# Optimization experiments

Measured on AMD Instinct MI355X. Metric: run time of the kernel, lower is better.

Reference implementation:

```python
import jax, jax.numpy as jnp
import numpy as np

N = 50000
E = 800000
IN_FEAT = 128
HEADS = 2
HEAD_DIM = 64  # hidden_feat // num_heads for 'concat'
HIDDEN = HEADS * HEAD_DIM
N_CLASSES = 16
NEG_SLOPE = 0.2
BN_EPS = 1e-5


def setup_inputs() -> dict:
    key = jax.random.key(0)
    ks = jax.random.split(key, 20)
    s = 0.1  # weight scale for numerical sanity
    return {
        "x": jax.random.normal(ks[0], (N, IN_FEAT), jnp.float32),
        "src0": jax.random.randint(ks[1], (E,), 0, N, jnp.int32),
        "dst0": jax.random.randint(ks[2], (E,), 0, N, jnp.int32),
        "ew0": jax.random.uniform(ks[3], (E,), jnp.float32),
        "src1": jax.random.randint(ks[4], (E,), 0, N, jnp.int32),
        "dst1": jax.random.randint(ks[5], (E,), 0, N, jnp.int32),
        "ew1": jax.random.uniform(ks[6], (E,), jnp.float32),
        "fc_w0": jax.random.normal(ks[7], (HIDDEN, IN_FEAT), jnp.float32) * s,
        "bias0": jnp.zeros((HIDDEN,), jnp.float32),
        "attn_l0": jax.random.normal(ks[8], (HEADS, HEAD_DIM), jnp.float32) * s,
        "attn_r0": jax.random.normal(ks[9], (HEADS, HEAD_DIM), jnp.float32) * s,
        "fc_w1": jax.random.normal(ks[10], (HIDDEN, IN_FEAT), jnp.float32) * s,
        "bias1": jnp.zeros((HIDDEN,), jnp.float32),
        "attn_l1": jax.random.normal(ks[11], (HEADS, HEAD_DIM), jnp.float32) * s,
        "attn_r1": jax.random.normal(ks[12], (HEADS, HEAD_DIM), jnp.float32) * s,
        "skip_w": jax.random.normal(ks[13], (HIDDEN, IN_FEAT), jnp.float32) * s,
        "skip_b": jnp.zeros((HIDDEN,), jnp.float32),
        "bn_gamma": jnp.ones((HIDDEN,), jnp.float32),
        "bn_beta": jnp.zeros((HIDDEN,), jnp.float32),
        "clf_w": jax.random.normal(ks[14], (N_CLASSES, HIDDEN), jnp.float32) * s,
        "clf_b": jnp.zeros((N_CLASSES,), jnp.float32),
    }


def _weighted_gat(x, src, dst, ew, fc_w, bias, attn_l, attn_r):
    # DGL GATConv with per-edge weight scaling of attention.
    f = (x @ fc_w.T).reshape(N, HEADS, HEAD_DIM)          # [N,H,D]
    el = jnp.sum(f * attn_l, axis=-1)                      # [N,H]
    er = jnp.sum(f * attn_r, axis=-1)                      # [N,H]
    e = jax.nn.leaky_relu(el[src] + er[dst], NEG_SLOPE)    # [E,H]
    # edge softmax over incoming edges of each dst, numerically stable
    m = jax.ops.segment_max(e, dst, num_segments=N)        # [N,H]
    ex = jnp.exp(e - m[dst])
    den = jax.ops.segment_sum(ex, dst, num_segments=N)     # [N,H]
    alpha = ex / den[dst]                                  # [E,H]
    alpha = alpha * ew[:, None]                            # edge-weight scaling
    msg = alpha[..., None] * f[src]                        # [E,H,D]
    out = jax.ops.segment_sum(msg, dst, num_segments=N)    # [N,H,D]
    return out + bias.reshape(1, HEADS, HEAD_DIM)


def reference(x, src0, dst0, ew0, src1, dst1, ew1,
              fc_w0, bias0, attn_l0, attn_r0,
              fc_w1, bias1, attn_l1, attn_r1,
              skip_w, skip_b, bn_gamma, bn_beta, clf_w, clf_b):
    # HeteroGraphConv with aggregate='sum': sum per-relation GAT outputs
    h2 = _weighted_gat(x, src0, dst0, ew0, fc_w0, bias0, attn_l0, attn_r0) \
       + _weighted_gat(x, src1, dst1, ew1, fc_w1, bias1, attn_l1, attn_r1)
    # multihead 'concat' aggregate with relu: flatten heads
    h2 = jax.nn.relu(h2).reshape(N, HIDDEN)
    # linear skip + residual add (dropout is identity at eval)
    h = (x @ skip_w.T + skip_b) + h2
    # classifier: BatchNorm1d (batch stats) -> ReLU -> Linear
    mu = jnp.mean(h, axis=0)
    var = jnp.mean((h - mu) ** 2, axis=0)
    hn = (h - mu) * jax.lax.rsqrt(var + BN_EPS) * bn_gamma + bn_beta
    logits = jax.nn.relu(hn) @ clf_w.T + clf_b
    return logits
```

## Files before the change

### kernel.cpp

```cpp
#include <hip/hip_runtime.h>
#include <hip/hip_bf16.h>

#define N_NODES 50000
#define N_EDGES 800000
#define HID 128
#define NEG_SLOPE 0.2f
#define BN_EPS 1e-5f

#define NBLK 256
#define BINSZ 512
#define BINSH 9
#define NBINS 98

typedef __bf16 v8bf __attribute__((ext_vector_type(8)));
typedef float v4f __attribute__((ext_vector_type(4)));

__device__ __forceinline__ float leaky(float v) {
    return (v > 0.f) ? v : v * NEG_SLOPE;
}
__device__ __forceinline__ unsigned int f2bu(float f) {
    __hip_bfloat16 b = __float2bfloat16(f);
    return (unsigned int)*reinterpret_cast<unsigned short*>(&b);
}
__device__ __forceinline__ unsigned int pack2bf(float lo, float hi) {
    return f2bu(lo) | (f2bu(hi) << 16);
}

__global__ __launch_bounds__(256) void k_prepw(const float* __restrict__ w0,
                                               const float* __restrict__ w1,
                                               const float* __restrict__ wsk,
                                               unsigned short* __restrict__ wb) {
    const int WQ = 128 * 128 / 4;
    int q = blockIdx.x * 256 + threadIdx.x;
    if (q >= 3 * WQ) return;
    int mat = q >> 12;
    int rem = q & 4095;
    const float* W = (mat == 0) ? w0 : (mat == 1) ? w1 : wsk;
    float4 v = ((const float4*)W)[rem];
    ushort4 o;
    o.x = (unsigned short)f2bu(v.x);
    o.y = (unsigned short)f2bu(v.y);
    o.z = (unsigned short)f2bu(v.z);
    o.w = (unsigned short)f2bu(v.w);
    *(ushort4*)(wb + (size_t)mat * 16384 + rem * 4) = o;
}

__global__ __launch_bounds__(256) void k_bincount(const int* __restrict__ dst0,
                                                  const int* __restrict__ dst1,
                                                  int* __restrict__ bincnt) {
    int rel = blockIdx.y;
    const int* dst = rel ? dst1 : dst0;
    __shared__ int cnt[NBINS];
    for (int i = threadIdx.x; i < NBINS; i += 256) cnt[i] = 0;
    __syncthreads();
    const int CH = (N_EDGES + NBLK - 1) / NBLK;
    int b0 = blockIdx.x * CH;
    int b1 = min(N_EDGES, b0 + CH);
    for (int e = b0 + threadIdx.x; e < b1; e += 256)
        atomicAdd(&cnt[dst[e] >> BINSH], 1);
    __syncthreads();
    for (int i = threadIdx.x; i < NBINS; i += 256)
        bincnt[rel * NBINS * NBLK + i * NBLK + blockIdx.x] = cnt[i];
}

__global__ __launch_bounds__(1024) void k_binscan(int* __restrict__ bincnt) {
    int* a = bincnt + blockIdx.x * NBINS * NBLK;
    const int TOT = NBINS * NBLK;
    const int CH = (TOT + 1023) / 1024;
    int tid = threadIdx.x;
    int base = tid * CH;
    int lv[CH];
    int sum = 0;
    for (int i = 0; i < CH; i++) {
        int idx = base + i;
        int v = (idx < TOT) ? a[idx] : 0;
        lv[i] = sum;
        sum += v;
    }
    __shared__ int ls[1024];
    ls[tid] = sum;
    __syncthreads();
    for (int ofs = 1; ofs < 1024; ofs <<= 1) {
        int v = (tid >= ofs) ? ls[tid - ofs] : 0;
        __syncthreads();
        ls[tid] += v;
        __syncthreads();
    }
    int pre = tid ? ls[tid - 1] : 0;
    for (int i = 0; i < CH; i++) {
        int idx = base + i;
        if (idx < TOT) a[idx] = pre + lv[i];
    }
}

__global__ __launch_bounds__(256) void k_binscatter(const int* __restrict__ dst0,
                                                    const int* __restrict__ dst1,
                                                    const int* __restrict__ src0,
                                                    const int* __restrict__ src1,
                                                    const float* __restrict__ ew0,
                                                    const float* __restrict__ ew1,
                                                    const int* __restrict__ bincnt,
                                                    int2* __restrict__ pairs0,
                                                    int2* __restrict__ pairs1) {
    int rel = blockIdx.y;
    const int* dst = rel ? dst1 : dst0;
    const int* src = rel ? src1 : src0;
    const float* ew = rel ? ew1 : ew0;
    int2* pairs = rel ? pairs1 : pairs0;
    __shared__ int cur[NBINS];
    for (int i = threadIdx.x; i < NBINS; i += 256)
        cur[i] = bincnt[rel * NBINS * NBLK + i * NBLK + blockIdx.x];
    __syncthreads();
    const int CH = (N_EDGES + NBLK - 1) / NBLK;
    int b0 = blockIdx.x * CH;
    int b1 = min(N_EDGES, b0 + CH);
    for (int e = b0 + threadIdx.x; e < b1; e += 256) {
        int d = dst[e];
        int pos = atomicAdd(&cur[d >> BINSH], 1);
        unsigned int packed = (unsigned int)(d & (BINSZ - 1)) |
                              ((unsigned int)src[e] << BINSH);
        pairs[pos] = make_int2((int)packed, __float_as_int(ew[e]));
    }
}

__global__ __launch_bounds__(256) void k_csr(const int* __restrict__ bincnt,
                                             const int2* __restrict__ pairs0,
                                             const int2* __restrict__ pairs1,
                                             const float* __restrict__ el0,
                                             const float* __restrict__ el1,
                                             int* __restrict__ offs0,
                                             int* __restrict__ offs1,
                                             int4* __restrict__ rec0,
                                             int4* __restrict__ rec1) {
    int rel = blockIdx.y;
    const int2* pairs = rel ? pairs1 : pairs0;
    const float* el = rel ? el1 : el0;
    int* offs = rel ? offs1 : offs0;
    int4* rec = rel ? rec1 : rec0;
    int bin = blockIdx.x;
    int tid = threadIdx.x;
    const int* bc = bincnt + rel * NBINS * NBLK;
    int pbase = bc[bin * NBLK];
    int pend = (bin < NBINS - 1) ? bc[(bin + 1) * NBLK] : N_EDGES;
    int n0 = bin << BINSH;
    int nn = min(N_NODES - n0, BINSZ);

    __shared__ int s_deg[BINSZ];
    __shared__ int s_ts[256];
    for (int i = tid; i < BINSZ; i += 256) s_deg[i] = 0;
    __syncthreads();
    for (int p = pbase + tid; p < pend; p += 256)
        atomicAdd(&s_deg[((unsigned int)pairs[p].x) & (BINSZ - 1)], 1);
    __syncthreads();

    int d0 = s_deg[tid * 2], d1 = s_deg[tid * 2 + 1];
    s_ts[tid] = d0 + d1;
    __syncthreads();
    for (int ofs = 1; ofs < 256; ofs <<= 1) {
        int v = (tid >= ofs) ? s_ts[tid - ofs] : 0;
        __syncthreads();
        s_ts[tid] += v;
        __syncthreads();
    }
    int pre = tid ? s_ts[tid - 1] : 0;
    s_deg[tid * 2] = pbase + pre;
    s_deg[tid * 2 + 1] = pbase + pre + d0;
    __syncthreads();

    for (int l = tid; l < nn; l += 256) offs[n0 + l] = s_deg[l];
    if (bin == NBINS - 1 && tid == 0) offs[N_NODES] = N_EDGES;
    __syncthreads();

    for (int p = pbase + tid; p < pend; p += 256) {
        int2 pr = pairs[p];
        unsigned int u = (unsigned int)pr.x;
        int dl = (int)(u & (BINSZ - 1));
        int s = (int)(u >> BINSH);
        int pos = atomicAdd(&s_deg[dl], 1);
        float2 ev = *(const float2*)(el + 2 * s);
        rec[pos] = make_int4(s << 8, pr.y,
                             __float_as_int(ev.x), __float_as_int(ev.y));
    }
}

__global__ __launch_bounds__(256) void k_gemm_mfma(
    const float* __restrict__ x, const unsigned short* __restrict__ wb,
    const float* __restrict__ skip_b,
    const float* __restrict__ al0, const float* __restrict__ ar0,
    const float* __restrict__ al1, const float* __restrict__ ar1,
    unsigned short* __restrict__ fb0, unsigned short* __restrict__ fb1,
    float* __restrict__ el0, float* __restrict__ er0,
    float* __restrict__ el1, float* __restrict__ er1,
    float* __restrict__ hs) {
    __shared__ unsigned short As[64][128];
    __shared__ unsigned short Bs[64][128];
    int tid = threadIdx.x;
    int m0 = blockIdx.x * 64;

#pragma unroll
    for (int i = 0; i < 4; i++) {
        int idx = tid * 4 + i;
        int row = idx >> 4, seg = idx & 15;
        int gr = m0 + row;
        uint4 o = make_uint4(0, 0, 0, 0);
        if (gr < N_NODES) {
            const float* p = x + (size_t)gr * HID + seg * 8;
            float4 p0 = *(const float4*)p;
            float4 p1 = *(const float4*)(p + 4);
            o.x = pack2bf(p0.x, p0.y);
            o.y = pack2bf(p0.z, p0.w);
            o.z = pack2bf(p1.x, p1.y);
            o.w = pack2bf(p1.z, p1.w);
        }
        *(uint4*)(&As[row][(seg ^ (row & 7)) * 8]) = o;
    }
    __syncthreads();

    int w = tid >> 6, l = tid & 63;
    int lr = l & 15, lg = l >> 4;
    int arow = w * 16 + lr;
    v8bf afrag[4];
#pragma unroll
    for (int kb = 0; kb < 4; kb++)
        afrag[kb] = *(v8bf*)(&As[arow][((kb * 4 + lg) ^ (arow & 7)) * 8]);

    for (int s = 0; s < 6; s++) {
        int mat = s >> 1;
        int j0 = (s & 1) * 64;
        const unsigned short* wmat = wb + (size_t)mat * 16384 + j0 * HID;
        __syncthreads();
#pragma unroll
        for (int i = 0; i < 4; i++) {
            int idx = tid * 4 + i;
            int row = idx >> 4, seg = idx & 15;
            uint4 wv = *(const uint4*)(wmat + row * HID + seg * 8);
            *(uint4*)(&Bs[row][(seg ^ (row & 7)) * 8]) = wv;
        }
        __syncthreads();

        v4f acc[4] = {};
#pragma unroll
        for (int nt = 0; nt < 4; nt++) {
            int brow = nt * 16 + lr;
#pragma unroll
            for (int kb = 0; kb < 4; kb++) {
                v8bf bfrag =
                    *(v8bf*)(&Bs[brow][((kb * 4 + lg) ^ (brow & 7)) * 8]);
                acc[nt] = __builtin_amdgcn_mfma_f32_16x16x32_bf16(
                    afrag[kb], bfrag, acc[nt], 0, 0, 0);
            }
        }

        if (mat < 2) {
            int h = s & 1;
            const float* al = mat ? al1 : al0;
            const float* ar = mat ? ar1 : ar0;
            float* elp = mat ? el1 : el0;
            float* erp = mat ? er1 : er0;
            unsigned short* fbp = mat ? fb1 : fb0;
            float elv[4] = {0.f, 0.f, 0.f, 0.f};
            float erv[4] = {0.f, 0.f, 0.f, 0.f};
#pragma unroll
            for (int nt = 0; nt < 4; nt++) {
                int colg = j0 + nt * 16 + lr;
                float av = al[colg], rv = ar[colg];
#pragma unroll
                for (int r = 0; r < 4; r++) {
                    elv[r] += acc[nt][r] * av;
                    erv[r] += acc[nt][r] * rv;
                }
            }
#pragma unroll
            for (int m = 1; m < 16; m <<= 1)
#pragma unroll
                for (int r = 0; r < 4; r++) {
                    elv[r] += __shfl_xor(elv[r], m);
                    erv[r] += __shfl_xor(erv[r], m);
                }
#pragma unroll
            for (int r = 0; r < 4; r++) {
                int grow = m0 + w * 16 + lg * 4 + r;
                if (grow >= N_NODES) continue;
#pragma unroll
                for (int nt = 0; nt < 4; nt++) {
                    int colg = j0 + nt * 16 + lr;
                    fbp[(size_t)grow * HID + colg] =
                        (unsigned short)f2bu(acc[nt][r]);
                }
                if (lr == 0) {
                    elp[grow * 2 + h] = elv[r];
                    erp[grow * 2 + h] = erv[r];
                }
            }
        } else {
#pragma unroll
            for (int r = 0; r < 4; r++) {
                int grow = m0 + w * 16 + lg * 4 + r;
                if (grow >= N_NODES) continue;
#pragma unroll
                for (int nt = 0; nt < 4; nt++) {
                    int colg = j0 + nt * 16 + lr;
                    hs[(size_t)grow * HID + colg] = acc[nt][r] + skip_b[colg];
                }
            }
        }
    }
}

__device__ __forceinline__ void agg_rel2(const int* __restrict__ offs,
                                         const int4* __restrict__ rec,
                                         const float* __restrict__ er,
                                         const unsigned char* __restrict__ fbb,
                                         int n, int lane, int sub,
                                         int hh, float* a) {
    int b = offs[n];
    int e_end = offs[n + 1];
    int deg = e_end - b;
    if (deg <= 0) return;
    float ern0 = er[2 * n], ern1 = er[2 * n + 1];

    const int NC = 4;
    int cs[NC];
    float cw0[NC], cw1[NC];
    unsigned int cpk[NC];
    float d0 = 0.f, d1 = 0.f;
    int nchunk = (deg + 63) >> 6;
    for (int ch = 0; ch < nchunk; ch++) {
        int p = b + (ch << 6) + lane;
        int s = 0;
        float w0 = 0.f, w1 = 0.f;
        if (p < e_end) {
            int4 r = rec[p];
            s = r.x;
            float wgt = __int_as_float(r.y);
            float x0 = expf(leaky(__int_as_float(r.z) + ern0));
            float x1 = expf(leaky(__int_as_float(r.w) + ern1));
            d0 += x0;
            d1 += x1;
            w0 = x0 * wgt;
            w1 = x1 * wgt;
        }
        if (ch < NC) {
            cs[ch] = s;
            cw0[ch] = w0;
            cw1[ch] = w1;
        }
    }
#pragma unroll
    for (int m = 32; m; m >>= 1) {
        d0 += __shfl_xor(d0, m);
        d1 += __shfl_xor(d1, m);
    }
    float inv0 = 1.f / d0, inv1 = 1.f / d1;
#pragma unroll
    for (int ch = 0; ch < NC; ch++)
        cpk[ch] = pack2bf(cw0[ch] * inv0, cw1[ch] * inv1);

    for (int ch = 0; ch < nchunk; ch++) {
        int s;
        unsigned int pk;
        if (ch < NC) {
            s = cs[ch];
            pk = cpk[ch];
        } else {
            int p = b + (ch << 6) + lane;
            s = 0;
            pk = 0;
            if (p < e_end) {
                int4 r = rec[p];
                s = r.x;
                float wgt = __int_as_float(r.y);
                float w0 = expf(leaky(__int_as_float(r.z) + ern0)) * wgt;
                float w1 = expf(leaky(__int_as_float(r.w) + ern1)) * wgt;
                pk = pack2bf(w0 * inv0, w1 * inv1);
            }
        }
        int cnt = deg - (ch << 6);
        if (cnt > 64) cnt = 64;
        int ng = (cnt + 3) >> 2;
#pragma unroll 2
        for (int g = 0; g < ng; g++) {
            int sl = (g << 2) + sub;
            int sj = __shfl(s, sl);
            unsigned int pkj = (unsigned int)__shfl((int)pk, sl);
            float aj = __uint_as_float(hh ? (pkj & 0xffff0000u) : (pkj << 16));
            uint4 fv = *(const uint4*)(fbb + sj);
            a[0] += aj * __uint_as_float(fv.x << 16);
            a[1] += aj * __uint_as_float(fv.x & 0xffff0000u);
            a[2] += aj * __uint_as_float(fv.y << 16);
            a[3] += aj * __uint_as_float(fv.y & 0xffff0000u);
            a[4] += aj * __uint_as_float(fv.z << 16);
            a[5] += aj * __uint_as_float(fv.z & 0xffff0000u);
            a[6] += aj * __uint_as_float(fv.w << 16);
            a[7] += aj * __uint_as_float(fv.w & 0xffff0000u);
        }
    }
}

__global__ __launch_bounds__(256) void k_aggregate(
    const int* __restrict__ offs0, const int4* __restrict__ rec0,
    const float* __restrict__ er0, const unsigned short* __restrict__ fb0,
    const int* __restrict__ offs1, const int4* __restrict__ rec1,
    const float* __restrict__ er1, const unsigned short* __restrict__ fb1,
    const float* __restrict__ bias0, const float* __restrict__ bias1,
    float* __restrict__ h) {
    int wave = threadIdx.x >> 6, lane = threadIdx.x & 63;
    int n = blockIdx.x * 4 + wave;
    if (n >= N_NODES) return;
    int cb = lane & 15;
    int sub = lane >> 4;
    int hh = cb >> 3;
    float a[8] = {0.f, 0.f, 0.f, 0.f, 0.f, 0.f, 0.f, 0.f};
    const unsigned char* fbb0 = (const unsigned char*)fb0 + cb * 16;
    const unsigned char* fbb1 = (const unsigned char*)fb1 + cb * 16;
    agg_rel2(offs0, rec0, er0, fbb0, n, lane, sub, hh, a);
    agg_rel2(offs1, rec1, er1, fbb1, n, lane, sub, hh, a);
#pragma unroll
    for (int j = 0; j < 8; j++) {
        a[j] += __shfl_xor(a[j], 16);
        a[j] += __shfl_xor(a[j], 32);
    }
    if (sub == 0) {
        size_t base = (size_t)n * HID + cb * 8;
        float4 v0 = *(const float4*)(h + base);
        float4 v1 = *(const float4*)(h + base + 4);
        int c0 = cb * 8;
        float4 o0, o1;
        o0.x = v0.x + fmaxf(a[0] + bias0[c0 + 0] + bias1[c0 + 0], 0.f);
        o0.y = v0.y + fmaxf(a[1] + bias0[c0 + 1] + bias1[c0 + 1], 0.f);
        o0.z = v0.z + fmaxf(a[2] + bias0[c0 + 2] + bias1[c0 + 2], 0.f);
        o0.w = v0.w + fmaxf(a[3] + bias0[c0 + 3] + bias1[c0 + 3], 0.f);
        o1.x = v1.x + fmaxf(a[4] + bias0[c0 + 4] + bias1[c0 + 4], 0.f);
        o1.y = v1.y + fmaxf(a[5] + bias0[c0 + 5] + bias1[c0 + 5], 0.f);
        o1.z = v1.z + fmaxf(a[6] + bias0[c0 + 6] + bias1[c0 + 6], 0.f);
        o1.w = v1.w + fmaxf(a[7] + bias0[c0 + 7] + bias1[c0 + 7], 0.f);
        *(float4*)(h + base) = o0;
        *(float4*)(h + base + 4) = o1;
    }
}

__global__ __launch_bounds__(256) void k_bnstats(const float* __restrict__ h,
                                                 double* __restrict__ psum,
                                                 double* __restrict__ psumsq) {
    int tid = threadIdx.x;
    const float4* h4 = (const float4*)h;
    double s[4] = {0.0, 0.0, 0.0, 0.0};
    double q[4] = {0.0, 0.0, 0.0, 0.0};
    const int totalv = N_NODES * HID / 4;
    const int stride = 512 * 256;
    for (int i = blockIdx.x * 256 + tid; i < totalv; i += stride) {
        float4 v = h4[i];
        s[0] += v.x; q[0] += (double)v.x * v.x;
        s[1] += v.y; q[1] += (double)v.y * v.y;
        s[2] += v.z; q[2] += (double)v.z * v.z;
        s[3] += v.w; q[3] += (double)v.w * v.w;
    }
    __shared__ double ls[256][4], lq[256][4];
#pragma unroll
    for (int j = 0; j < 4; j++) {
        ls[tid][j] = s[j];
        lq[tid][j] = q[j];
    }
    __syncthreads();
    if (tid < 32) {
#pragma unroll
        for (int j = 0; j < 4; j++) {
            double ss = 0.0, qq = 0.0;
            for (int t = tid; t < 256; t += 32) {
                ss += ls[t][j];
                qq += lq[t][j];
            }
            psum[blockIdx.x * 128 + tid * 4 + j] = ss;
            psumsq[blockIdx.x * 128 + tid * 4 + j] = qq;
        }
    }
}

__global__ void k_bn_finalize(const double* __restrict__ psum,
                              const double* __restrict__ psumsq,
                              const float* __restrict__ gamma,
                              const float* __restrict__ beta,
                              float* __restrict__ ss) {
    int c = threadIdx.x;
    double s = 0.0, q = 0.0;
    for (int b = 0; b < 512; b++) {
        s += psum[b * 128 + c];
        q += psumsq[b * 128 + c];
    }
    double mu = s / N_NODES;
    double var = q / N_NODES - mu * mu;
    float sc = gamma[c] * (float)(1.0 / sqrt(var + (double)BN_EPS));
    ss[c] = sc;
    ss[128 + c] = beta[c] - (float)mu * sc;
}

__global__ __launch_bounds__(256) void k_classify(const float* __restrict__ h,
                                                  const float* __restrict__ ss,
                                                  const float* __restrict__ clf_w,
                                                  const float* __restrict__ clf_b,
                                                  float* __restrict__ out) {
    int w = threadIdx.x >> 6, l = threadIdx.x & 63;
    int lr = l & 15, lg = l >> 4;
    int n0 = (blockIdx.x * 4 + w) * 16;
    if (n0 >= N_NODES) return;

    v8bf afrag[4], bfrag[4];
#pragma unroll
    for (int kb = 0; kb < 4; kb++) {
        int k0 = kb * 32 + lg * 8;
        const float* bp = clf_w + lr * HID + k0;
        float4 b0 = *(const float4*)bp;
        float4 b1 = *(const float4*)(bp + 4);
        bfrag[kb][0] = (__bf16)b0.x; bfrag[kb][1] = (__bf16)b0.y;
        bfrag[kb][2] = (__bf16)b0.z; bfrag[kb][3] = (__bf16)b0.w;
        bfrag[kb][4] = (__bf16)b1.x; bfrag[kb][5] = (__bf16)b1.y;
        bfrag[kb][6] = (__bf16)b1.z; bfrag[kb][7] = (__bf16)b1.w;
        const float* ap = h + (size_t)(n0 + lr) * HID + k0;
        float4 a0 = *(const float4*)ap;
        float4 a1 = *(const float4*)(ap + 4);
        float4 sc0 = *(const float4*)(ss + k0);
        float4 sc1 = *(const float4*)(ss + k0 + 4);
        float4 sh0 = *(const float4*)(ss + 128 + k0);
        float4 sh1 = *(const float4*)(ss + 128 + k0 + 4);
        afrag[kb][0] = (__bf16)fmaxf(a0.x * sc0.x + sh0.x, 0.f);
        afrag[kb][1] = (__bf16)fmaxf(a0.y * sc0.y + sh0.y, 0.f);
        afrag[kb][2] = (__bf16)fmaxf(a0.z * sc0.z + sh0.z, 0.f);
        afrag[kb][3] = (__bf16)fmaxf(a0.w * sc0.w + sh0.w, 0.f);
        afrag[kb][4] = (__bf16)fmaxf(a1.x * sc1.x + sh1.x, 0.f);
        afrag[kb][5] = (__bf16)fmaxf(a1.y * sc1.y + sh1.y, 0.f);
        afrag[kb][6] = (__bf16)fmaxf(a1.z * sc1.z + sh1.z, 0.f);
        afrag[kb][7] = (__bf16)fmaxf(a1.w * sc1.w + sh1.w, 0.f);
    }
    v4f acc = {};
#pragma unroll
    for (int kb = 0; kb < 4; kb++)
        acc = __builtin_amdgcn_mfma_f32_16x16x32_bf16(afrag[kb], bfrag[kb],
                                                      acc, 0, 0, 0);
    float cb = clf_b[lr];
#pragma unroll
    for (int r = 0; r < 4; r++) {
        int n = n0 + lg * 4 + r;
        out[(size_t)n * 16 + lr] = acc[r] + cb;
    }
}

extern "C" void kernel_launch(void* const* d_in, const int* in_sizes, int n_in,
                              void* d_out, int out_size, void* d_ws, size_t ws_size,
                              hipStream_t stream) {
    (void)in_sizes; (void)n_in; (void)out_size; (void)ws_size;
    const float* x      = (const float*)d_in[0];
    const int*   src0   = (const int*)d_in[1];
    const int*   dst0   = (const int*)d_in[2];
    const float* ew0    = (const float*)d_in[3];
    const int*   src1   = (const int*)d_in[4];
    const int*   dst1   = (const int*)d_in[5];
    const float* ew1    = (const float*)d_in[6];
    const float* fc_w0  = (const float*)d_in[7];
    const float* bias0  = (const float*)d_in[8];
    const float* al0    = (const float*)d_in[9];
    const float* ar0    = (const float*)d_in[10];
    const float* fc_w1  = (const float*)d_in[11];
    const float* bias1  = (const float*)d_in[12];
    const float* al1    = (const float*)d_in[13];
    const float* ar1    = (const float*)d_in[14];
    const float* skip_w = (const float*)d_in[15];
    const float* skip_b = (const float*)d_in[16];
    const float* gamma  = (const float*)d_in[17];
    const float* beta   = (const float*)d_in[18];
    const float* clf_w  = (const float*)d_in[19];
    const float* clf_b  = (const float*)d_in[20];
    float* out = (float*)d_out;

    char* wsp = (char*)d_ws;
    size_t off = 0;
    auto alloc = [&](size_t bytes) -> char* {
        char* p = wsp + off;
        off += (bytes + 255) & ~(size_t)255;
        return p;
    };
    unsigned short* wbf = (unsigned short*)alloc((size_t)3 * 16384 * 2);
    unsigned short* fb0 = (unsigned short*)alloc((size_t)N_NODES * HID * 2);
    unsigned short* fb1 = (unsigned short*)alloc((size_t)N_NODES * HID * 2);
    float*  hs     = (float*)alloc((size_t)N_NODES * HID * 4);
    float*  el0    = (float*)alloc((size_t)N_NODES * 2 * 4);
    float*  er0    = (float*)alloc((size_t)N_NODES * 2 * 4);
    float*  el1    = (float*)alloc((size_t)N_NODES * 2 * 4);
    float*  er1    = (float*)alloc((size_t)N_NODES * 2 * 4);
    int*    bincnt = (int*)alloc((size_t)2 * NBINS * NBLK * 4);
    int2*   pairs0 = (int2*)alloc((size_t)N_EDGES * 8);
    int2*   pairs1 = (int2*)alloc((size_t)N_EDGES * 8);
    int*    offs0  = (int*)alloc((size_t)(N_NODES + 1) * 4);
    int*    offs1  = (int*)alloc((size_t)(N_NODES + 1) * 4);
    int4*   rec0   = (int4*)alloc((size_t)N_EDGES * 16);
    int4*   rec1   = (int4*)alloc((size_t)N_EDGES * 16);
    double* psum   = (double*)alloc((size_t)512 * 128 * 8);
    double* psumsq = (double*)alloc((size_t)512 * 128 * 8);
    float*  ss     = (float*)alloc(256 * 4);

    k_prepw<<<48, 256, 0, stream>>>(fc_w0, fc_w1, skip_w, wbf);

    dim3 gbin(NBLK, 2);
    k_bincount<<<gbin, 256, 0, stream>>>(dst0, dst1, bincnt);
    k_binscan<<<2, 1024, 0, stream>>>(bincnt);
    k_binscatter<<<gbin, 256, 0, stream>>>(dst0, dst1, src0, src1, ew0, ew1,
                                           bincnt, pairs0, pairs1);

    k_gemm_mfma<<<(N_NODES + 63) / 64, 256, 0, stream>>>(
        x, wbf, skip_b, al0, ar0, al1, ar1,
        fb0, fb1, el0, er0, el1, er1, hs);

    dim3 gcsr(NBINS, 2);
    k_csr<<<gcsr, 256, 0, stream>>>(bincnt, pairs0, pairs1, el0, el1,
                                    offs0, offs1, rec0, rec1);

    k_aggregate<<<(N_NODES + 3) / 4, 256, 0, stream>>>(
        offs0, rec0, er0, fb0, offs1, rec1, er1, fb1, bias0, bias1, hs);

    k_bnstats<<<512, 256, 0, stream>>>(hs, psum, psumsq);
    k_bn_finalize<<<1, 128, 0, stream>>>(psum, psumsq, gamma, beta, ss);
    k_classify<<<(N_NODES + 63) / 64, 256, 0, stream>>>(
        hs, ss, clf_w, clf_b, out);
}
```

Baseline: 221.4 us.

## Transpose MFMA outputs for vectorized stores and widen aggregation gathers to 32 bytes

```diff
diff --git a/kernel.cpp b/kernel.cpp
--- a/kernel.cpp
+++ b/kernel.cpp
@@ -218,6 +218,8 @@
 
     int w = tid >> 6, l = tid & 63;
     int lr = l & 15, lg = l >> 4;
+    int node = m0 + w * 16 + lr;
+    bool valid = node < N_NODES;
     int arow = w * 16 + lr;
     v8bf afrag[4];
 #pragma unroll
@@ -247,7 +249,7 @@
                 v8bf bfrag =
                     *(v8bf*)(&Bs[brow][((kb * 4 + lg) ^ (brow & 7)) * 8]);
                 acc[nt] = __builtin_amdgcn_mfma_f32_16x16x32_bf16(
-                    afrag[kb], bfrag, acc[nt], 0, 0, 0);
+                    bfrag, afrag[kb], acc[nt], 0, 0, 0);
             }
         }
 
@@ -258,50 +260,45 @@
             float* elp = mat ? el1 : el0;
             float* erp = mat ? er1 : er0;
             unsigned short* fbp = mat ? fb1 : fb0;
-            float elv[4] = {0.f, 0.f, 0.f, 0.f};
-            float erv[4] = {0.f, 0.f, 0.f, 0.f};
+            float elv = 0.f, erv = 0.f;
 #pragma unroll
             for (int nt = 0; nt < 4; nt++) {
-                int colg = j0 + nt * 16 + lr;
-                float av = al[colg], rv = ar[colg];
-#pragma unroll
-                for (int r = 0; r < 4; r++) {
-                    elv[r] += acc[nt][r] * av;
-                    erv[r] += acc[nt][r] * rv;
+                int c0 = j0 + nt * 16 + lg * 4;
+                float4 av = *(const float4*)(al + c0);
+                float4 rv = *(const float4*)(ar + c0);
+                elv += acc[nt][0] * av.x + acc[nt][1] * av.y +
+                       acc[nt][2] * av.z + acc[nt][3] * av.w;
+                erv += acc[nt][0] * rv.x + acc[nt][1] * rv.y +
+                       acc[nt][2] * rv.z + acc[nt][3] * rv.w;
+            }
+            elv += __shfl_xor(elv, 16);
+            elv += __shfl_xor(elv, 32);
+            erv += __shfl_xor(erv, 16);
+            erv += __shfl_xor(erv, 32);
+            if (valid) {
+#pragma unroll
+                for (int nt = 0; nt < 4; nt++) {
+                    uint2 o;
+                    o.x = pack2bf(acc[nt][0], acc[nt][1]);
+                    o.y = pack2bf(acc[nt][2], acc[nt][3]);
+                    *(uint2*)(fbp + (size_t)node * HID + j0 + nt * 16 + lg * 4) = o;
+                }
+                if (lg == 0) {
+                    elp[node * 2 + h] = elv;
+                    erp[node * 2 + h] = erv;
                 }
             }
-#pragma unroll
-            for (int m = 1; m < 16; m <<= 1)
-#pragma unroll
-                for (int r = 0; r < 4; r++) {
-                    elv[r] += __shfl_xor(elv[r], m);
-                    erv[r] += __shfl_xor(erv[r], m);
-                }
-#pragma unroll
-            for (int r = 0; r < 4; r++) {
-                int grow = m0 + w * 16 + lg * 4 + r;
-                if (grow >= N_NODES) continue;
-#pragma unroll
-                for (int nt = 0; nt < 4; nt++) {
-                    int colg = j0 + nt * 16 + lr;
-                    fbp[(size_t)grow * HID + colg] =
-                        (unsigned short)f2bu(acc[nt][r]);
-                }
-                if (lr == 0) {
-                    elp[grow * 2 + h] = elv[r];
-                    erp[grow * 2 + h] = erv[r];
-                }
-            }
-        } else {
-#pragma unroll
-            for (int r = 0; r < 4; r++) {
-                int grow = m0 + w * 16 + lg * 4 + r;
-                if (grow >= N_NODES) continue;
-#pragma unroll
-                for (int nt = 0; nt < 4; nt++) {
-                    int colg = j0 + nt * 16 + lr;
-                    hs[(size_t)grow * HID + colg] = acc[nt][r] + skip_b[colg];
-                }
+        } else if (valid) {
+#pragma unroll
+            for (int nt = 0; nt < 4; nt++) {
+                int c0 = j0 + nt * 16 + lg * 4;
+                float4 sb = *(const float4*)(skip_b + c0);
+                float4 o;
+                o.x = acc[nt][0] + sb.x;
+                o.y = acc[nt][1] + sb.y;
+                o.z = acc[nt][2] + sb.z;
+                o.w = acc[nt][3] + sb.w;
+                *(float4*)(hs + (size_t)node * HID + c0) = o;
             }
         }
     }
@@ -311,7 +308,7 @@
                                          const int4* __restrict__ rec,
                                          const float* __restrict__ er,
                                          const unsigned char* __restrict__ fbb,
-                                         int n, int lane, int sub,
+                                         int n, int lane, int sub8,
                                          int hh, float* a) {
     int b = offs[n];
     int e_end = offs[n + 1];
@@ -377,22 +374,31 @@
         }
         int cnt = deg - (ch << 6);
         if (cnt > 64) cnt = 64;
-        int ng = (cnt + 3) >> 2;
+        int ng = (cnt + 7) >> 3;
 #pragma unroll 2
         for (int g = 0; g < ng; g++) {
-            int sl = (g << 2) + sub;
+            int sl = (g << 3) + sub8;
             int sj = __shfl(s, sl);
             unsigned int pkj = (unsigned int)__shfl((int)pk, sl);
             float aj = __uint_as_float(hh ? (pkj & 0xffff0000u) : (pkj << 16));
-            uint4 fv = *(const uint4*)(fbb + sj);
-            a[0] += aj * __uint_as_float(fv.x << 16);
-            a[1] += aj * __uint_as_float(fv.x & 0xffff0000u);
-            a[2] += aj * __uint_as_float(fv.y << 16);
-            a[3] += aj * __uint_as_float(fv.y & 0xffff0000u);
-            a[4] += aj * __uint_as_float(fv.z << 16);
-            a[5] += aj * __uint_as_float(fv.z & 0xffff0000u);
-            a[6] += aj * __uint_as_float(fv.w << 16);
-            a[7] += aj * __uint_as_float(fv.w & 0xffff0000u);
+            uint4 f0 = *(const uint4*)(fbb + sj);
+            uint4 f1 = *(const uint4*)(fbb + sj + 16);
+            a[0]  += aj * __uint_as_float(f0.x << 16);
+            a[1]  += aj * __uint_as_float(f0.x & 0xffff0000u);
+            a[2]  += aj * __uint_as_float(f0.y << 16);
+            a[3]  += aj * __uint_as_float(f0.y & 0xffff0000u);
+            a[4]  += aj * __uint_as_float(f0.z << 16);
+            a[5]  += aj * __uint_as_float(f0.z & 0xffff0000u);
+            a[6]  += aj * __uint_as_float(f0.w << 16);
+            a[7]  += aj * __uint_as_float(f0.w & 0xffff0000u);
+            a[8]  += aj * __uint_as_float(f1.x << 16);
+            a[9]  += aj * __uint_as_float(f1.x & 0xffff0000u);
+            a[10] += aj * __uint_as_float(f1.y << 16);
+            a[11] += aj * __uint_as_float(f1.y & 0xffff0000u);
+            a[12] += aj * __uint_as_float(f1.z << 16);
+            a[13] += aj * __uint_as_float(f1.z & 0xffff0000u);
+            a[14] += aj * __uint_as_float(f1.w << 16);
+            a[15] += aj * __uint_as_float(f1.w & 0xffff0000u);
         }
     }
 }
@@ -407,35 +413,35 @@
     int wave = threadIdx.x >> 6, lane = threadIdx.x & 63;
     int n = blockIdx.x * 4 + wave;
     if (n >= N_NODES) return;
-    int cb = lane & 15;
-    int sub = lane >> 4;
-    int hh = cb >> 3;
-    float a[8] = {0.f, 0.f, 0.f, 0.f, 0.f, 0.f, 0.f, 0.f};
-    const unsigned char* fbb0 = (const unsigned char*)fb0 + cb * 16;
-    const unsigned char* fbb1 = (const unsigned char*)fb1 + cb * 16;
-    agg_rel2(offs0, rec0, er0, fbb0, n, lane, sub, hh, a);
-    agg_rel2(offs1, rec1, er1, fbb1, n, lane, sub, hh, a);
-#pragma unroll
-    for (int j = 0; j < 8; j++) {
+    int cb8 = lane & 7;
+    int sub8 = lane >> 3;
+    int hh = cb8 >> 2;
+    float a[16] = {};
+    const unsigned char* fbb0 = (const unsigned char*)fb0 + cb8 * 32;
+    const unsigned char* fbb1 = (const unsigned char*)fb1 + cb8 * 32;
+    agg_rel2(offs0, rec0, er0, fbb0, n, lane, sub8, hh, a);
+    agg_rel2(offs1, rec1, er1, fbb1, n, lane, sub8, hh, a);
+#pragma unroll
+    for (int j = 0; j < 16; j++) {
+        a[j] += __shfl_xor(a[j], 8);
         a[j] += __shfl_xor(a[j], 16);
         a[j] += __shfl_xor(a[j], 32);
     }
-    if (sub == 0) {
-        size_t base = (size_t)n * HID + cb * 8;
-        float4 v0 = *(const float4*)(h + base);
-        float4 v1 = *(const float4*)(h + base + 4);
-        int c0 = cb * 8;
-        float4 o0, o1;
-        o0.x = v0.x + fmaxf(a[0] + bias0[c0 + 0] + bias1[c0 + 0], 0.f);
-        o0.y = v0.y + fmaxf(a[1] + bias0[c0 + 1] + bias1[c0 + 1], 0.f);
-        o0.z = v0.z + fmaxf(a[2] + bias0[c0 + 2] + bias1[c0 + 2], 0.f);
-        o0.w = v0.w + fmaxf(a[3] + bias0[c0 + 3] + bias1[c0 + 3], 0.f);
-        o1.x = v1.x + fmaxf(a[4] + bias0[c0 + 4] + bias1[c0 + 4], 0.f);
-        o1.y = v1.y + fmaxf(a[5] + bias0[c0 + 5] + bias1[c0 + 5], 0.f);
-        o1.z = v1.z + fmaxf(a[6] + bias0[c0 + 6] + bias1[c0 + 6], 0.f);
-        o1.w = v1.w + fmaxf(a[7] + bias0[c0 + 7] + bias1[c0 + 7], 0.f);
-        *(float4*)(h + base) = o0;
-        *(float4*)(h + base + 4) = o1;
+    if (sub8 == 0) {
+        int c0 = cb8 * 16;
+        size_t base = (size_t)n * HID + c0;
+#pragma unroll
+        for (int q = 0; q < 4; q++) {
+            float4 v = *(const float4*)(h + base + q * 4);
+            float4 b0 = *(const float4*)(bias0 + c0 + q * 4);
+            float4 b1 = *(const float4*)(bias1 + c0 + q * 4);
+            float4 o;
+            o.x = v.x + fmaxf(a[q * 4 + 0] + b0.x + b1.x, 0.f);
+            o.y = v.y + fmaxf(a[q * 4 + 1] + b0.y + b1.y, 0.f);
+            o.z = v.z + fmaxf(a[q * 4 + 2] + b0.z + b1.z, 0.f);
+            o.w = v.w + fmaxf(a[q * 4 + 3] + b0.w + b1.w, 0.f);
+            *(float4*)(h + base + q * 4) = o;
+        }
     }
 }
 
@@ -534,14 +540,15 @@
     v4f acc = {};
 #pragma unroll
     for (int kb = 0; kb < 4; kb++)
-        acc = __builtin_amdgcn_mfma_f32_16x16x32_bf16(afrag[kb], bfrag[kb],
+        acc = __builtin_amdgcn_mfma_f32_16x16x32_bf16(bfrag[kb], afrag[kb],
                                                       acc, 0, 0, 0);
-    float cb = clf_b[lr];
-#pragma unroll
-    for (int r = 0; r < 4; r++) {
-        int n = n0 + lg * 4 + r;
-        out[(size_t)n * 16 + lr] = acc[r] + cb;
-    }
+    float4 cb = *(const float4*)(clf_b + lg * 4);
+    float4 o;
+    o.x = acc[0] + cb.x;
+    o.y = acc[1] + cb.y;
+    o.z = acc[2] + cb.z;
+    o.w = acc[3] + cb.w;
+    *(float4*)(out + (size_t)(n0 + lr) * 16 + lg * 4) = o;
 }
 
 extern "C" void kernel_launch(void* const* d_in, const int* in_sizes, int n_in,
```

Result: slower. 231.2 us (+4.4%).
